# Kernel tuning notes

Hardware: AMD Instinct MI355X
Metric: run time of the kernel (lower is better)

The kernel has to match this reference:

```python
import jax, jax.numpy as jnp
import numpy as np


def setup_inputs() -> dict:
    key = jax.random.key(0)
    k1, k2, k3 = jax.random.split(key, 3)
    W, H = 512, 512
    num_neurons = (W - 1) * (H - 1)
    x = jax.random.normal(k1, (16, 16, W, H), dtype=jnp.float32)
    weights = jax.random.uniform(k2, (num_neurons, 4), dtype=jnp.float32)
    bias = jax.random.uniform(k3, (num_neurons,), dtype=jnp.float32)
    return {"x": x, "weights": weights, "bias": bias}


def reference(x, weights, bias):
    # x: [B, C, W, H]; locally-connected 2x2 conv with unshared per-position
    # weights. Original loops run w in [1, W-2], h in [1, H-2], so output
    # row 0 and column 0 (of the (W-1, H-1) output) remain zero.
    B, C, W, H = x.shape
    # 2x2 patch at output position (w, h) is x[w-1:w+1, h-1:h+1], reshaped
    # row-major to 4 elements: (w-1,h-1), (w-1,h), (w,h-1), (w,h).
    patches = jnp.stack(
        [
            x[:, :, 0:W - 2, 0:H - 2],
            x[:, :, 0:W - 2, 1:H - 1],
            x[:, :, 1:W - 1, 0:H - 2],
            x[:, :, 1:W - 1, 1:H - 1],
        ],
        axis=-1,
    )  # [B, C, W-2, H-2, 4]
    wi = jnp.arange(1, W - 1)  # [W-2]
    hi = jnp.arange(1, H - 1)  # [H-2]
    idx = (W - 1) * wi[:, None] + hi[None, :]  # neuron index per position
    w_sel = weights[idx]  # [W-2, H-2, 4]
    b_sel = bias[idx]     # [W-2, H-2]
    core = jnp.einsum("bcwhk,whk->bcwh", patches, w_sel) + b_sel
    out = jnp.zeros((B, C, W - 1, H - 1), dtype=x.dtype)
    out = out.at[:, :, 1:, 1:].set(core)
    return out
```

## Files before the change

### kernel.cpp

```cpp
#include <hip/hip_runtime.h>


typedef float f4u __attribute__((ext_vector_type(4), aligned(4)));
typedef float f2u __attribute__((ext_vector_type(2), aligned(4)));

constexpr int PLANE_OUT = 511 * 511;
constexpr int PLANE_IN  = 512 * 512;
constexpr int PSTRIDE   = 8;

__global__ __launch_bounds__(256, 6)
void lc_conv2x2_v13(const float* __restrict__ x,
                    const float4* __restrict__ weights,
                    const float* __restrict__ bias,
                    float* __restrict__ out, int planes) {
    const int q = blockIdx.x;
    const int b = blockIdx.y;
    const int t = threadIdx.x;

    if (b == 255) {
        if (t != 0) return;
        const float4 wt = weights[PLANE_OUT - 1];
        const float  bv = bias[PLANE_OUT - 1];
        for (int p = q; p < planes; p += PSTRIDE) {
            const float* xp = x + (size_t)p * PLANE_IN;
            float v = xp[509 * 512 + 509] * wt.x + xp[509 * 512 + 510] * wt.y
                    + xp[510 * 512 + 509] * wt.z + xp[510 * 512 + 510] * wt.w + bv;
            out[(size_t)p * PLANE_OUT + (PLANE_OUT - 1)] = v;
        }
        return;
    }

    const int o0 = (b << 10) | (t << 2);
    const int w  = o0 / 511;
    const int h  = o0 - w * 511;

    bool cj[4], zj[4];
    #pragma unroll
    for (int j = 0; j < 4; ++j) {
        const int hr = h + j;
        cj[j] = (hr >= 511);
        const int wj = w + (cj[j] ? 1 : 0);
        const int hj = hr - (cj[j] ? 511 : 0);
        zj[j] = (wj == 0) || (hj == 0);
    }

    float4 wtr[4];
    #pragma unroll
    for (int j = 0; j < 4; ++j) wtr[j] = weights[o0 + j];
    const f4u bv4 = *(const f4u*)(bias + o0);

    int tb = o0 + w - 513;
    if (tb < 0) tb = 0;
    const int bb = tb + 512;

    #pragma unroll 4
    for (int p = q; p < planes; p += PSTRIDE) {
        const float* xp = x + (size_t)p * PLANE_IN;

        f4u T0 = *(const f4u*)(xp + tb);
        f2u T1 = *(const f2u*)(xp + tb + 4);
        f4u B0 = *(const f4u*)(xp + bb);
        f2u B1 = *(const f2u*)(xp + bb + 4);
        const float tv[6] = {T0.x, T0.y, T0.z, T0.w, T1.x, T1.y};
        const float bv[6] = {B0.x, B0.y, B0.z, B0.w, B1.x, B1.y};

        f4u r;
        #pragma unroll
        for (int j = 0; j < 4; ++j) {
            const float xtl = cj[j] ? tv[j + 1] : tv[j];
            const float xtr = cj[j] ? tv[j + 2] : tv[j + 1];
            const float xbl = cj[j] ? bv[j + 1] : bv[j];
            const float xbr = cj[j] ? bv[j + 2] : bv[j + 1];
            const float v = xtl * wtr[j].x + xtr * wtr[j].y
                          + xbl * wtr[j].z + xbr * wtr[j].w + bv4[j];
            r[j] = zj[j] ? 0.0f : v;
        }
        __builtin_nontemporal_store(r, (f4u*)(out + (size_t)p * PLANE_OUT + o0));
    }
}

extern "C" void kernel_launch(void* const* d_in, const int* in_sizes, int n_in,
                              void* d_out, int out_size, void* d_ws, size_t ws_size,
                              hipStream_t stream) {
    const float*  x       = (const float*)d_in[0];
    const float4* weights = (const float4*)d_in[1];
    const float*  bias    = (const float*)d_in[2];
    float*        out     = (float*)d_out;

    int planes = in_sizes[0] / PLANE_IN;
    dim3 grid(PSTRIDE, 256);
    lc_conv2x2_v13<<<grid, 256, 0, stream>>>(x, weights, bias, out, planes);
}
```

Baseline: 117.4 us.

## Process 8 outputs per thread with contiguous plane chunks and pre-zeroed border weights

```diff
diff --git a/kernel.cpp b/kernel.cpp
--- a/kernel.cpp
+++ b/kernel.cpp
@@ -6,10 +6,9 @@
 
 constexpr int PLANE_OUT = 511 * 511;
 constexpr int PLANE_IN  = 512 * 512;
-constexpr int PSTRIDE   = 8;
 
-__global__ __launch_bounds__(256, 6)
-void lc_conv2x2_v13(const float* __restrict__ x,
+__global__ __launch_bounds__(256, 7)
+void lc_conv2x2_v19(const float* __restrict__ x,
                     const float4* __restrict__ weights,
                     const float* __restrict__ bias,
                     float* __restrict__ out, int planes) {
@@ -17,65 +16,98 @@
     const int b = blockIdx.y;
     const int t = threadIdx.x;
 
-    if (b == 255) {
-        if (t != 0) return;
+    const int chunk = planes >> 4;
+    const int p0 = (q & 7) * 2 * chunk + (q >> 3) * chunk;
+
+    const int o0 = (b << 11) | (t << 3);
+    if (o0 > PLANE_OUT - 1) return;
+
+    if (o0 == PLANE_OUT - 1) {
         const float4 wt = weights[PLANE_OUT - 1];
         const float  bv = bias[PLANE_OUT - 1];
-        for (int p = q; p < planes; p += PSTRIDE) {
-            const float* xp = x + (size_t)p * PLANE_IN;
+        for (int i = 0; i < chunk; ++i) {
+            const float* xp = x + (size_t)(p0 + i) * PLANE_IN;
             float v = xp[509 * 512 + 509] * wt.x + xp[509 * 512 + 510] * wt.y
                     + xp[510 * 512 + 509] * wt.z + xp[510 * 512 + 510] * wt.w + bv;
-            out[(size_t)p * PLANE_OUT + (PLANE_OUT - 1)] = v;
+            out[(size_t)(p0 + i) * PLANE_OUT + (PLANE_OUT - 1)] = v;
         }
         return;
     }
 
-    const int o0 = (b << 10) | (t << 2);
+    if (o0 <= 504) {
+        const f4u z = {0.0f, 0.0f, 0.0f, 0.0f};
+        for (int i = 0; i < chunk; ++i) {
+            float* op = out + (size_t)(p0 + i) * PLANE_OUT + o0;
+            __builtin_nontemporal_store(z, (f4u*)op);
+            __builtin_nontemporal_store(z, (f4u*)(op + 4));
+        }
+        return;
+    }
+
     const int w  = o0 / 511;
     const int h  = o0 - w * 511;
-
-    bool cj[4], zj[4];
-    #pragma unroll
-    for (int j = 0; j < 4; ++j) {
-        const int hr = h + j;
-        cj[j] = (hr >= 511);
-        const int wj = w + (cj[j] ? 1 : 0);
-        const int hj = hr - (cj[j] ? 511 : 0);
-        zj[j] = (wj == 0) || (hj == 0);
-    }
-
-    float4 wtr[4];
-    #pragma unroll
-    for (int j = 0; j < 4; ++j) wtr[j] = weights[o0 + j];
-    const f4u bv4 = *(const f4u*)(bias + o0);
-
-    int tb = o0 + w - 513;
-    if (tb < 0) tb = 0;
+    const int tb = o0 + w - 513;
     const int bb = tb + 512;
 
+    bool cj[8];
+    #pragma unroll
+    for (int j = 0; j < 8; ++j) cj[j] = (h + j >= 511);
+
+    float wX[8], wY[8], wZ[8], wW[8], bR[8];
+    const f4u ba = *(const f4u*)(bias + o0);
+    const f4u bb4 = *(const f4u*)(bias + o0 + 4);
+    const float braw[8] = {ba.x, ba.y, ba.z, ba.w, bb4.x, bb4.y, bb4.z, bb4.w};
+    #pragma unroll
+    for (int j = 0; j < 8; ++j) {
+        const bool border = (h + j == 511) || (h + j == 0);
+        const float4 wt = weights[o0 + j];
+        wX[j] = border ? 0.0f : wt.x;
+        wY[j] = border ? 0.0f : wt.y;
+        wZ[j] = border ? 0.0f : wt.z;
+        wW[j] = border ? 0.0f : wt.w;
+        bR[j] = border ? 0.0f : braw[j];
+    }
+    asm volatile(""
+        : "+v"(wX[0]), "+v"(wX[1]), "+v"(wX[2]), "+v"(wX[3]),
+          "+v"(wX[4]), "+v"(wX[5]), "+v"(wX[6]), "+v"(wX[7]),
+          "+v"(wY[0]), "+v"(wY[1]), "+v"(wY[2]), "+v"(wY[3]),
+          "+v"(wY[4]), "+v"(wY[5]), "+v"(wY[6]), "+v"(wY[7]),
+          "+v"(bR[0]), "+v"(bR[1]), "+v"(bR[2]), "+v"(bR[3]));
+    asm volatile(""
+        : "+v"(wZ[0]), "+v"(wZ[1]), "+v"(wZ[2]), "+v"(wZ[3]),
+          "+v"(wZ[4]), "+v"(wZ[5]), "+v"(wZ[6]), "+v"(wZ[7]),
+          "+v"(wW[0]), "+v"(wW[1]), "+v"(wW[2]), "+v"(wW[3]),
+          "+v"(wW[4]), "+v"(wW[5]), "+v"(wW[6]), "+v"(wW[7]),
+          "+v"(bR[4]), "+v"(bR[5]), "+v"(bR[6]), "+v"(bR[7]));
+
     #pragma unroll 4
-    for (int p = q; p < planes; p += PSTRIDE) {
+    for (int i = 0; i < chunk; ++i) {
+        const int p = p0 + i;
         const float* xp = x + (size_t)p * PLANE_IN;
 
         f4u T0 = *(const f4u*)(xp + tb);
-        f2u T1 = *(const f2u*)(xp + tb + 4);
+        f4u T1 = *(const f4u*)(xp + tb + 4);
+        f2u T2 = *(const f2u*)(xp + tb + 8);
         f4u B0 = *(const f4u*)(xp + bb);
-        f2u B1 = *(const f2u*)(xp + bb + 4);
-        const float tv[6] = {T0.x, T0.y, T0.z, T0.w, T1.x, T1.y};
-        const float bv[6] = {B0.x, B0.y, B0.z, B0.w, B1.x, B1.y};
+        f4u B1 = *(const f4u*)(xp + bb + 4);
+        f2u B2 = *(const f2u*)(xp + bb + 8);
+        const float tv[10] = {T0.x, T0.y, T0.z, T0.w, T1.x, T1.y, T1.z, T1.w, T2.x, T2.y};
+        const float bw[10] = {B0.x, B0.y, B0.z, B0.w, B1.x, B1.y, B1.z, B1.w, B2.x, B2.y};
 
-        f4u r;
+        f4u r0, r1;
         #pragma unroll
-        for (int j = 0; j < 4; ++j) {
+        for (int j = 0; j < 8; ++j) {
             const float xtl = cj[j] ? tv[j + 1] : tv[j];
             const float xtr = cj[j] ? tv[j + 2] : tv[j + 1];
-            const float xbl = cj[j] ? bv[j + 1] : bv[j];
-            const float xbr = cj[j] ? bv[j + 2] : bv[j + 1];
-            const float v = xtl * wtr[j].x + xtr * wtr[j].y
-                          + xbl * wtr[j].z + xbr * wtr[j].w + bv4[j];
-            r[j] = zj[j] ? 0.0f : v;
+            const float xbl = cj[j] ? bw[j + 1] : bw[j];
+            const float xbr = cj[j] ? bw[j + 2] : bw[j + 1];
+            const float v = xtl * wX[j] + xtr * wY[j]
+                          + xbl * wZ[j] + xbr * wW[j] + bR[j];
+            if (j < 4) r0[j] = v; else r1[j - 4] = v;
         }
-        __builtin_nontemporal_store(r, (f4u*)(out + (size_t)p * PLANE_OUT + o0));
+        float* op = out + (size_t)p * PLANE_OUT + o0;
+        __builtin_nontemporal_store(r0, (f4u*)op);
+        __builtin_nontemporal_store(r1, (f4u*)(op + 4));
     }
 }
 
@@ -88,6 +120,6 @@
     float*        out     = (float*)d_out;
 
     int planes = in_sizes[0] / PLANE_IN;
-    dim3 grid(PSTRIDE, 256);
-    lc_conv2x2_v13<<<grid, 256, 0, stream>>>(x, weights, bias, out, planes);
+    dim3 grid(16, 128);
+    lc_conv2x2_v19<<<grid, 256, 0, stream>>>(x, weights, bias, out, planes);
 }
```

Result: slower. 175.9 us (+49.8%).
